# Kernel optimization log

Measured on AMD Instinct MI355X. Metric: run time of the kernel, lower is better.

## Reference

```python
import jax, jax.numpy as jnp
import numpy as np

NEG_SLOPE = 0.2  # PyG GATConv default negative_slope


def gat_conv(x, edge_index, W, a_src, a_dst, bias, heads, out_ch, concat):
    """PyG-style GATConv (eval mode, add_self_loops=True).
    x: [N, F_in], edge_index: [2, E] (row 0 = src, row 1 = dst).
    """
    N = x.shape[0]
    loop = jnp.arange(N, dtype=edge_index.dtype)
    src = jnp.concatenate([edge_index[0], loop])  # [E+N]
    dst = jnp.concatenate([edge_index[1], loop])

    h = (x @ W).reshape(N, heads, out_ch)            # [N, H, C]
    alpha_s = jnp.einsum('nhc,hc->nh', h, a_src)     # [N, H]
    alpha_d = jnp.einsum('nhc,hc->nh', h, a_dst)

    e = jax.nn.leaky_relu(alpha_s[src] + alpha_d[dst], NEG_SLOPE)  # [E+N, H]
    # softmax over incoming edges per destination node (numerically stable)
    m = jax.ops.segment_max(e, dst, num_segments=N)                # [N, H]
    ex = jnp.exp(e - m[dst])
    denom = jax.ops.segment_sum(ex, dst, num_segments=N)
    alpha = ex / (denom[dst] + 1e-16)                              # [E+N, H]

    msg = h[src] * alpha[:, :, None]                               # [E+N, H, C]
    out = jax.ops.segment_sum(msg, dst, num_segments=N)            # [N, H, C]
    out = out.reshape(N, heads * out_ch) if concat else out.mean(axis=1)
    return out + bias


def setup_inputs() -> dict:
    key = jax.random.key(0)
    ks = jax.random.split(key, 10)
    N, F_in, H, C1, LAT, E = 10000, 2000, 10, 128, 64, 150000
    hid = H * C1  # 1280
    x = jax.random.normal(ks[0], (N, F_in), dtype=jnp.float32)
    edge_index = jax.random.randint(ks[1], (2, E), 0, N, dtype=jnp.int64)
    # layer 1 params (glorot-ish scaling)
    W1 = jax.random.normal(ks[2], (F_in, H * C1), dtype=jnp.float32) * (1.0 / np.sqrt(F_in))
    a_src1 = jax.random.normal(ks[3], (H, C1), dtype=jnp.float32) * 0.1
    a_dst1 = jax.random.normal(ks[4], (H, C1), dtype=jnp.float32) * 0.1
    b1 = jnp.zeros((hid,), dtype=jnp.float32)
    # layer 2 params
    W2 = jax.random.normal(ks[5], (hid, H * LAT), dtype=jnp.float32) * (1.0 / np.sqrt(hid))
    a_src2 = jax.random.normal(ks[6], (H, LAT), dtype=jnp.float32) * 0.1
    a_dst2 = jax.random.normal(ks[7], (H, LAT), dtype=jnp.float32) * 0.1
    b2 = jnp.zeros((LAT,), dtype=jnp.float32)
    return {"x": x, "edge_index": edge_index,
            "W1": W1, "a_src1": a_src1, "a_dst1": a_dst1, "b1": b1,
            "W2": W2, "a_src2": a_src2, "a_dst2": a_dst2, "b2": b2}


def reference(x, edge_index, W1, a_src1, a_dst1, b1, W2, a_src2, a_dst2, b2):
    H, C1, LAT = 10, 128, 64
    h1 = gat_conv(x, edge_index, W1, a_src1, a_dst1, b1, H, C1, concat=True)
    h1 = jax.nn.relu(h1)
    h2 = gat_conv(h1, edge_index, W2, a_src2, a_dst2, b2, H, LAT, concat=False)
    return jax.nn.relu(h2)
```

## Files before the change

### kernel.cpp

```cpp
#include <hip/hip_runtime.h>

#define NN    10000
#define FIN   2000
#define NH    10
#define C1    128
#define C2    64
#define HC1   1280
#define HC2   640
#define MP    10240
#define K1P   2016
#define CAP   96

typedef _Float16 f16x8 __attribute__((ext_vector_type(8)));
typedef _Float16 f16x4 __attribute__((ext_vector_type(4)));
typedef _Float16 f16x2 __attribute__((ext_vector_type(2)));
typedef float    f32x4 __attribute__((ext_vector_type(4)));

__device__ __forceinline__ float leaky(float x) { return x > 0.f ? x : 0.2f * x; }

#define NCAST (2 * MP)
#define NW1   (63 * 40)
__global__ void k_prep(const float* __restrict__ x, _Float16* __restrict__ A1,
                       const float* __restrict__ W1, _Float16* __restrict__ W1t) {
    __shared__ float tile[32][33];
    int bid = blockIdx.x, t = threadIdx.x;
    if (bid < NCAST) {
        int r = bid >> 1;
        int c = (bid & 1) * 256 + t;
        if (c >= K1P / 4) return;
        float4 v = make_float4(0.f, 0.f, 0.f, 0.f);
        if (r < NN && c < FIN / 4) v = *(const float4*)(x + (long)r * FIN + 4 * c);
        f16x4 o = {(_Float16)v.x, (_Float16)v.y, (_Float16)v.z, (_Float16)v.w};
        *(f16x4*)(A1 + (long)r * K1P + 4 * c) = o;
        return;
    }
    int i = bid - NCAST;
    int kbase = (i % 63) * 32, nbase = (i / 63) * 32;
    int tx = t & 31, ty = t >> 5;
#pragma unroll
    for (int j = 0; j < 4; j++) {
        int k = kbase + ty + j * 8;
        float v = (k < FIN) ? W1[(long)k * HC1 + nbase + tx] : 0.0f;
        tile[ty + j * 8][tx] = v;
    }
    __syncthreads();
#pragma unroll
    for (int j = 0; j < 4; j++) {
        int n = nbase + ty + j * 8;
        W1t[(long)n * K1P + kbase + tx] = (_Float16)tile[tx][ty + j * 8];
    }
}

__device__ __forceinline__ void gl2lds16(const void* g, void* l) {
    __builtin_amdgcn_global_load_lds((const __attribute__((address_space(1))) void*)g,
                                     (__attribute__((address_space(3))) void*)l, 16, 0, 0);
}

__global__ __launch_bounds__(512, 2) void k_gemm1(const _Float16* __restrict__ A,
                                                  const _Float16* __restrict__ Bt,
                                                  _Float16* __restrict__ C,
                                                  const float* __restrict__ asf,
                                                  const float* __restrict__ adf,
                                                  float* __restrict__ as,
                                                  float* __restrict__ ad,
                                                  const float* __restrict__ W2,
                                                  _Float16* __restrict__ W2t,
                                                  const int* __restrict__ ei,
                                                  int* __restrict__ cnt,
                                                  int* __restrict__ bucket,
                                                  int E, int nblk, int fillb) {
    constexpr int K    = K1P;
    constexpr int N    = HC1;
    constexpr int TBUF = 256 * 32;
    __shared__ char smem[3 * TBUF * 2 * 2] __attribute__((aligned(16)));
    _Float16* As = (_Float16*)smem;
    _Float16* Bs = (_Float16*)(smem + 3 * TBUF * 2);

    int bid = blockIdx.x;
    int t = threadIdx.x;
    if (bid >= nblk) {
        int sb = bid - nblk;
        if (sb < fillb) {
            int i = sb * 512 + t;
            if (i < E + NN) {
                int s, d;
                if (i < E) { s = ei[i]; d = ei[E + i]; }
                else       { s = i - E; d = i - E; }
                int slot = atomicAdd(&cnt[d], 1);
                if (slot < CAP) bucket[d * CAP + slot] = s;
            }
            return;
        }
        int half = t >> 8, t256 = t & 255;
        int i2 = (sb - fillb) * 2 + half;
        int kbase = (i2 % 40) * 32, nbase = (i2 / 40) * 32;
        float* tile = (float*)smem + half * (32 * 33);
        int tx = t256 & 31, ty = t256 >> 5;
#pragma unroll
        for (int j = 0; j < 4; j++) {
            int k = kbase + ty + j * 8;
            tile[(ty + j * 8) * 33 + tx] = W2[(long)k * HC2 + nbase + tx];
        }
        __syncthreads();
#pragma unroll
        for (int j = 0; j < 4; j++) {
            int n = nbase + ty + j * 8;
            W2t[(long)n * HC1 + kbase + tx] = (_Float16)tile[tx * 33 + ty + j * 8];
        }
        return;
    }

    int r = bid & 7, qb = bid >> 3;
    int n_t = qb % 5;
    int m_t = r + 8 * (qb / 5);
    int m0 = m_t * 256;
    int n0 = n_t * 256;
    int lane = t & 63, wave = t >> 6;
    int wr = wave >> 2, wc = wave & 3;
    int lrow = lane & 15, q = lane >> 4;

    f32x4 acc[8][4] = {};

    int sS[2];
#pragma unroll
    for (int i = 0; i < 2; i++) sS[i] = t + 512 * i;
    const _Float16* Ar[2];
    const _Float16* Br[2];
#pragma unroll
    for (int i = 0; i < 2; i++) {
        int row = sS[i] >> 2, gq = (sS[i] & 3) ^ ((sS[i] >> 3) & 3);
        Ar[i] = A  + (long)(m0 + row) * K + gq * 8;
        Br[i] = Bt + (long)(n0 + row) * K + gq * 8;
    }

    int aoff[8], boff[4];
#pragma unroll
    for (int i = 0; i < 8; i++) {
        int rowa = wr * 128 + i * 16 + lrow;
        aoff[i] = rowa * 32 + ((q ^ ((rowa >> 1) & 3)) << 3);
    }
#pragma unroll
    for (int i = 0; i < 4; i++) {
        int rowb = wc * 64 + i * 16 + lrow;
        boff[i] = rowb * 32 + ((q ^ ((rowb >> 1) & 3)) << 3);
    }

    auto stage = [&](int it, int buf) {
        int k0 = it << 5;
#pragma unroll
        for (int i = 0; i < 2; i++) gl2lds16(Ar[i] + k0, &As[buf * TBUF + sS[i] * 8]);
#pragma unroll
        for (int i = 0; i < 2; i++) gl2lds16(Br[i] + k0, &Bs[buf * TBUF + sS[i] * 8]);
    };

    constexpr int WVM = 0x0F70 | 4;
    int nk = K >> 5;
    stage(0, 0);
    stage(1, 1);
    int cur = 0;
    for (int it = 0; it < nk; it++) {
        if (it + 1 < nk) __builtin_amdgcn_s_waitcnt(WVM);
        else             __builtin_amdgcn_s_waitcnt(0x0F70);
        __builtin_amdgcn_s_barrier();
        int nxt = cur + 2; if (nxt >= 3) nxt -= 3;
        if (it + 2 < nk) stage(it + 2, nxt);

        f16x8 af[8], bf[4];
#pragma unroll
        for (int i = 0; i < 8; i++) af[i] = *(const f16x8*)&As[cur * TBUF + aoff[i]];
#pragma unroll
        for (int i = 0; i < 4; i++) bf[i] = *(const f16x8*)&Bs[cur * TBUF + boff[i]];
#pragma unroll
        for (int mt = 0; mt < 8; mt++)
#pragma unroll
            for (int nt = 0; nt < 4; nt++)
                acc[mt][nt] = __builtin_amdgcn_mfma_f32_16x16x32_f16(bf[nt], af[mt], acc[mt][nt], 0, 0, 0);
        cur = (cur + 1 == 3) ? 0 : cur + 1;
    }

#pragma unroll
    for (int mt = 0; mt < 8; mt++) {
        int m = m0 + wr * 128 + mt * 16 + lrow;
#pragma unroll
        for (int nt = 0; nt < 4; nt++) {
            int n = n0 + wc * 64 + nt * 16 + q * 4;
            f16x4 o = {(_Float16)acc[mt][nt][0], (_Float16)acc[mt][nt][1],
                       (_Float16)acc[mt][nt][2], (_Float16)acc[mt][nt][3]};
            *(f16x4*)(C + (long)m * N + n) = o;
        }
    }

    float4 av[4], dvv[4];
#pragma unroll
    for (int nt = 0; nt < 4; nt++) {
        av[nt]  = *(const float4*)(asf + n0 + wc * 64 + nt * 16 + q * 4);
        dvv[nt] = *(const float4*)(adf + n0 + wc * 64 + nt * 16 + q * 4);
    }
    __syncthreads();
    float* sAs = (float*)smem;
    float* sAd = (float*)smem + 1024;
#pragma unroll
    for (int mt = 0; mt < 8; mt++) {
        float ps = 0.f, pd = 0.f;
#pragma unroll
        for (int nt = 0; nt < 4; nt++) {
            ps += acc[mt][nt][0] * av[nt].x + acc[mt][nt][1] * av[nt].y
                + acc[mt][nt][2] * av[nt].z + acc[mt][nt][3] * av[nt].w;
            pd += acc[mt][nt][0] * dvv[nt].x + acc[mt][nt][1] * dvv[nt].y
                + acc[mt][nt][2] * dvv[nt].z + acc[mt][nt][3] * dvv[nt].w;
        }
        ps += __shfl_xor(ps, 16); ps += __shfl_xor(ps, 32);
        pd += __shfl_xor(pd, 16); pd += __shfl_xor(pd, 32);
        if (q == 0) {
            int rl = wr * 128 + mt * 16 + lrow;
            sAs[rl * 4 + wc] = ps;
            sAd[rl * 4 + wc] = pd;
        }
    }
    __syncthreads();
    if (t < 256) {
        int m = m0 + t;
        if (m < NN) {
            int hb = n0 >> 7;
            as[m * NH + hb]     = sAs[t * 4 + 0] + sAs[t * 4 + 1];
            as[m * NH + hb + 1] = sAs[t * 4 + 2] + sAs[t * 4 + 3];
            ad[m * NH + hb]     = sAd[t * 4 + 0] + sAd[t * 4 + 1];
            ad[m * NH + hb + 1] = sAd[t * 4 + 2] + sAd[t * 4 + 3];
        }
    }
}

template<int MFRAG>
__global__ __launch_bounds__(256, 3) void k_gemm(const _Float16* __restrict__ A,
                                                 const _Float16* __restrict__ Bt,
                                                 _Float16* __restrict__ C, int K, int N,
                                                 int NTN,
                                                 const float* __restrict__ asf,
                                                 const float* __restrict__ adf,
                                                 float* __restrict__ as,
                                                 float* __restrict__ ad,
                                                 int headw) {
    constexpr int BM   = MFRAG * 32;
    constexpr int ABUF = BM * 32;
    constexpr int ASL  = BM / 64;
    constexpr int WVM  = 0x0F70 | (ASL + 2);
    __shared__ char smem[3 * ABUF * 2 + 3 * 8192] __attribute__((aligned(16)));
    _Float16* As = (_Float16*)smem;
    _Float16* Bs = (_Float16*)(smem + 3 * ABUF * 2);

    int bid = blockIdx.x;
    int r = bid & 7, qb = bid >> 3;
    int n_t = qb % NTN;
    int m_t = r + 8 * (qb / NTN);
    int m0 = m_t * BM;
    int n0 = n_t * 128;
    int t = threadIdx.x;
    int lane = t & 63, wave = t >> 6;
    int wr = wave >> 1, wc = wave & 1;
    int lrow = lane & 15, q = lane >> 4;

    f32x4 acc[MFRAG][4] = {};

    int sA[ASL], sB[2];
#pragma unroll
    for (int i = 0; i < ASL; i++) sA[i] = t + 256 * i;
#pragma unroll
    for (int i = 0; i < 2; i++) sB[i] = t + 256 * i;
    const _Float16* Ar[ASL];
    const _Float16* Br[2];
#pragma unroll
    for (int i = 0; i < ASL; i++) {
        int row = sA[i] >> 2, gq = (sA[i] & 3) ^ ((sA[i] >> 3) & 3);
        Ar[i] = A + (long)(m0 + row) * K + gq * 8;
    }
#pragma unroll
    for (int i = 0; i < 2; i++) {
        int row = sB[i] >> 2, gq = (sB[i] & 3) ^ ((sB[i] >> 3) & 3);
        Br[i] = Bt + (long)(n0 + row) * K + gq * 8;
    }

    int aoff[MFRAG], boff[4];
#pragma unroll
    for (int i = 0; i < MFRAG; i++) {
        int rowa = wr * (MFRAG * 16) + i * 16 + lrow;
        aoff[i] = rowa * 32 + ((q ^ ((rowa >> 1) & 3)) << 3);
    }
#pragma unroll
    for (int i = 0; i < 4; i++) {
        int rowb = wc * 64 + i * 16 + lrow;
        boff[i] = rowb * 32 + ((q ^ ((rowb >> 1) & 3)) << 3);
    }

    auto stage = [&](int it, int buf) {
        int k0 = it << 5;
#pragma unroll
        for (int i = 0; i < ASL; i++) gl2lds16(Ar[i] + k0, &As[buf * ABUF + sA[i] * 8]);
#pragma unroll
        for (int i = 0; i < 2; i++) gl2lds16(Br[i] + k0, &Bs[buf * 4096 + sB[i] * 8]);
    };

    int nk = K >> 5;
    stage(0, 0);
    stage(1, 1);
    int cur = 0;
    for (int it = 0; it < nk; it++) {
        if (it + 1 < nk) __builtin_amdgcn_s_waitcnt(WVM);
        else             __builtin_amdgcn_s_waitcnt(0x0F70);
        __builtin_amdgcn_s_barrier();
        int nxt = cur + 2; if (nxt >= 3) nxt -= 3;
        if (it + 2 < nk) stage(it + 2, nxt);

        f16x8 af[MFRAG], bf[4];
#pragma unroll
        for (int i = 0; i < MFRAG; i++) af[i] = *(const f16x8*)&As[cur * ABUF + aoff[i]];
#pragma unroll
        for (int i = 0; i < 4; i++) bf[i] = *(const f16x8*)&Bs[cur * 4096 + boff[i]];
#pragma unroll
        for (int mt = 0; mt < MFRAG; mt++)
#pragma unroll
            for (int nt = 0; nt < 4; nt++)
                acc[mt][nt] = __builtin_amdgcn_mfma_f32_16x16x32_f16(bf[nt], af[mt], acc[mt][nt], 0, 0, 0);
        cur = (cur + 1 == 3) ? 0 : cur + 1;
    }

#pragma unroll
    for (int mt = 0; mt < MFRAG; mt++) {
        int m = m0 + wr * (MFRAG * 16) + mt * 16 + lrow;
#pragma unroll
        for (int nt = 0; nt < 4; nt++) {
            int n = n0 + wc * 64 + nt * 16 + q * 4;
            f16x4 o = {(_Float16)acc[mt][nt][0], (_Float16)acc[mt][nt][1],
                       (_Float16)acc[mt][nt][2], (_Float16)acc[mt][nt][3]};
            *(f16x4*)(C + (long)m * N + n) = o;
        }
    }

    float4 av[4], dvv[4];
#pragma unroll
    for (int nt = 0; nt < 4; nt++) {
        av[nt]  = *(const float4*)(asf + n0 + wc * 64 + nt * 16 + q * 4);
        dvv[nt] = *(const float4*)(adf + n0 + wc * 64 + nt * 16 + q * 4);
    }
    __syncthreads();
    float* sAs = (float*)smem;
    float* sAd = (float*)smem + BM * 2;
#pragma unroll
    for (int mt = 0; mt < MFRAG; mt++) {
        float ps = 0.f, pd = 0.f;
#pragma unroll
        for (int nt = 0; nt < 4; nt++) {
            ps += acc[mt][nt][0] * av[nt].x + acc[mt][nt][1] * av[nt].y
                + acc[mt][nt][2] * av[nt].z + acc[mt][nt][3] * av[nt].w;
            pd += acc[mt][nt][0] * dvv[nt].x + acc[mt][nt][1] * dvv[nt].y
                + acc[mt][nt][2] * dvv[nt].z + acc[mt][nt][3] * dvv[nt].w;
        }
        ps += __shfl_xor(ps, 16); ps += __shfl_xor(ps, 32);
        pd += __shfl_xor(pd, 16); pd += __shfl_xor(pd, 32);
        if (q == 0) {
            int rl = wr * (MFRAG * 16) + mt * 16 + lrow;
            sAs[rl * 2 + wc] = ps;
            sAd[rl * 2 + wc] = pd;
        }
    }
    __syncthreads();
    if (t < BM) {
        int m = m0 + t;
        if (m < NN) {
            int hb = n0 / headw;
            if (headw == 128) {
                as[m * NH + hb] = sAs[t * 2] + sAs[t * 2 + 1];
                ad[m * NH + hb] = sAd[t * 2] + sAd[t * 2 + 1];
            } else {
                as[m * NH + hb]     = sAs[t * 2];
                as[m * NH + hb + 1] = sAs[t * 2 + 1];
                ad[m * NH + hb]     = sAd[t * 2];
                ad[m * NH + hb + 1] = sAd[t * 2 + 1];
            }
        }
    }
}

__global__ __launch_bounds__(320) void k_agg1(const int* __restrict__ cnt,
                                              const int* __restrict__ bucket,
                                              const float* __restrict__ as,
                                              const float* __restrict__ ad,
                                              const _Float16* __restrict__ h,
                                              const float* __restrict__ bias,
                                              _Float16* __restrict__ A2) {
    __shared__ int sidx[64];
    __shared__ float sal[64 * NH];
    int n = blockIdx.x, t = threadIdx.x;
    if (n >= NN) {
        f16x4 z = {(_Float16)0.f, (_Float16)0.f, (_Float16)0.f, (_Float16)0.f};
        *(f16x4*)(A2 + (long)n * HC1 + 4 * t) = z;
        return;
    }
    int deg = min(cnt[n], CAP);
    const int* bkt = bucket + (long)n * CAP;
    int w = t >> 6, lane = t & 63;
    int hd = t >> 5;
    float acc[4] = {0, 0, 0, 0};

    if (deg <= 64) {
        int src = (lane < deg) ? bkt[lane] : 0;
        float2 adv = *(const float2*)(ad + n * NH + 2 * w);
        float x0 = 0.f, x1 = 0.f;
        if (lane < deg) {
            float2 avv = *(const float2*)(as + (long)src * NH + 2 * w);
            x0 = __expf(leaky(avv.x + adv.x));
            x1 = __expf(leaky(avv.y + adv.y));
        }
        float s0 = x0, s1 = x1;
        for (int m = 32; m; m >>= 1) {
            s0 += __shfl_xor(s0, m);
            s1 += __shfl_xor(s1, m);
        }
        if (lane < deg) {
            sal[lane * NH + 2 * w]     = x0 / (s0 + 1e-16f);
            sal[lane * NH + 2 * w + 1] = x1 / (s1 + 1e-16f);
            if (w == 0) sidx[lane] = src;
        }
        __syncthreads();
        int j = 0;
        for (; j + 8 <= deg; j += 8) {
            int sj[8]; float aa[8];
#pragma unroll
            for (int u = 0; u < 8; u++) { sj[u] = sidx[j + u]; aa[u] = sal[(j + u) * NH + hd]; }
            f16x4 vv[8];
#pragma unroll
            for (int u = 0; u < 8; u++) vv[u] = *(const f16x4*)(h + (long)sj[u] * HC1 + 4 * t);
#pragma unroll
            for (int i = 0; i < 4; i++) {
                float s = 0.f;
#pragma unroll
                for (int u = 0; u < 8; u++) s += aa[u] * (float)vv[u][i];
                acc[i] += s;
            }
        }
        for (; j + 4 <= deg; j += 4) {
            int sj0 = sidx[j], sj1 = sidx[j + 1], sj2 = sidx[j + 2], sj3 = sidx[j + 3];
            float a0 = sal[j * NH + hd], a1 = sal[(j + 1) * NH + hd];
            float a2 = sal[(j + 2) * NH + hd], a3 = sal[(j + 3) * NH + hd];
            f16x4 v0 = *(const f16x4*)(h + (long)sj0 * HC1 + 4 * t);
            f16x4 v1 = *(const f16x4*)(h + (long)sj1 * HC1 + 4 * t);
            f16x4 v2 = *(const f16x4*)(h + (long)sj2 * HC1 + 4 * t);
            f16x4 v3 = *(const f16x4*)(h + (long)sj3 * HC1 + 4 * t);
#pragma unroll
            for (int i = 0; i < 4; i++)
                acc[i] += a0 * (float)v0[i] + a1 * (float)v1[i]
                        + a2 * (float)v2[i] + a3 * (float)v3[i];
        }
        for (; j < deg; j++) {
            int src2 = sidx[j];
            float a = sal[j * NH + hd];
            f16x4 v = *(const f16x4*)(h + (long)src2 * HC1 + 4 * t);
#pragma unroll
            for (int i = 0; i < 4; i++) acc[i] += a * (float)v[i];
        }
    } else {
        float2 adv = *(const float2*)(ad + n * NH + 2 * w);
        float s0 = 0.f, s1 = 0.f;
        for (int j = lane; j < deg; j += 64) {
            float2 avv = *(const float2*)(as + (long)bkt[j] * NH + 2 * w);
            s0 += __expf(leaky(avv.x + adv.x));
            s1 += __expf(leaky(avv.y + adv.y));
        }
        for (int m = 32; m; m >>= 1) {
            s0 += __shfl_xor(s0, m);
            s1 += __shfl_xor(s1, m);
        }
        float i0 = 1.f / (s0 + 1e-16f), i1 = 1.f / (s1 + 1e-16f);
        for (int c0 = 0; c0 < deg; c0 += 64) {
            int cn = min(64, deg - c0);
            __syncthreads();
            if (lane < cn) {
                int src = bkt[c0 + lane];
                float2 avv = *(const float2*)(as + (long)src * NH + 2 * w);
                sal[lane * NH + 2 * w]     = __expf(leaky(avv.x + adv.x)) * i0;
                sal[lane * NH + 2 * w + 1] = __expf(leaky(avv.y + adv.y)) * i1;
                if (w == 0) sidx[lane] = src;
            }
            __syncthreads();
            for (int j = 0; j < cn; j++) {
                int src2 = sidx[j];
                float a = sal[j * NH + hd];
                f16x4 v = *(const f16x4*)(h + (long)src2 * HC1 + 4 * t);
#pragma unroll
                for (int i = 0; i < 4; i++) acc[i] += a * (float)v[i];
            }
        }
    }
    f16x4 o;
#pragma unroll
    for (int i = 0; i < 4; i++) {
        float x = acc[i] + bias[4 * t + i];
        o[i] = (_Float16)(x > 0.f ? x : 0.f);
    }
    *(f16x4*)(A2 + (long)n * HC1 + 4 * t) = o;
}

__global__ __launch_bounds__(320) void k_agg2(const int* __restrict__ cnt,
                                              const int* __restrict__ bucket,
                                              const float* __restrict__ as,
                                              const float* __restrict__ ad,
                                              const _Float16* __restrict__ h,
                                              const float* __restrict__ bias,
                                              float* __restrict__ out) {
    __shared__ int sidx[64];
    __shared__ float sal[64 * NH];
    __shared__ float facc[HC2];
    int n = blockIdx.x, t = threadIdx.x;
    int deg = min(cnt[n], CAP);
    const int* bkt = bucket + (long)n * CAP;
    int w = t >> 6, lane = t & 63;
    int hd = t >> 5;
    float a0 = 0.f, a1 = 0.f;

    if (deg <= 64) {
        int src = (lane < deg) ? bkt[lane] : 0;
        float2 adv = *(const float2*)(ad + n * NH + 2 * w);
        float x0 = 0.f, x1 = 0.f;
        if (lane < deg) {
            float2 avv = *(const float2*)(as + (long)src * NH + 2 * w);
            x0 = __expf(leaky(avv.x + adv.x));
            x1 = __expf(leaky(avv.y + adv.y));
        }
        float s0 = x0, s1 = x1;
        for (int m = 32; m; m >>= 1) {
            s0 += __shfl_xor(s0, m);
            s1 += __shfl_xor(s1, m);
        }
        if (lane < deg) {
            sal[lane * NH + 2 * w]     = x0 / (s0 + 1e-16f);
            sal[lane * NH + 2 * w + 1] = x1 / (s1 + 1e-16f);
            if (w == 0) sidx[lane] = src;
        }
        __syncthreads();
        int j = 0;
        for (; j + 8 <= deg; j += 8) {
            int sj[8]; float aa[8];
#pragma unroll
            for (int u = 0; u < 8; u++) { sj[u] = sidx[j + u]; aa[u] = sal[(j + u) * NH + hd]; }
            f16x2 vv[8];
#pragma unroll
            for (int u = 0; u < 8; u++) vv[u] = *(const f16x2*)(h + (long)sj[u] * HC2 + 2 * t);
            float p0 = 0.f, p1 = 0.f;
#pragma unroll
            for (int u = 0; u < 8; u++) { p0 += aa[u] * (float)vv[u][0]; p1 += aa[u] * (float)vv[u][1]; }
            a0 += p0; a1 += p1;
        }
        for (; j + 4 <= deg; j += 4) {
            int sj0 = sidx[j], sj1 = sidx[j + 1], sj2 = sidx[j + 2], sj3 = sidx[j + 3];
            float b0 = sal[j * NH + hd], b1 = sal[(j + 1) * NH + hd];
            float b2 = sal[(j + 2) * NH + hd], b3 = sal[(j + 3) * NH + hd];
            f16x2 v0 = *(const f16x2*)(h + (long)sj0 * HC2 + 2 * t);
            f16x2 v1 = *(const f16x2*)(h + (long)sj1 * HC2 + 2 * t);
            f16x2 v2 = *(const f16x2*)(h + (long)sj2 * HC2 + 2 * t);
            f16x2 v3 = *(const f16x2*)(h + (long)sj3 * HC2 + 2 * t);
            a0 += b0 * (float)v0[0] + b1 * (float)v1[0] + b2 * (float)v2[0] + b3 * (float)v3[0];
            a1 += b0 * (float)v0[1] + b1 * (float)v1[1] + b2 * (float)v2[1] + b3 * (float)v3[1];
        }
        for (; j < deg; j++) {
            int src2 = sidx[j];
            float a = sal[j * NH + hd];
            f16x2 v = *(const f16x2*)(h + (long)src2 * HC2 + 2 * t);
            a0 += a * (float)v[0];
            a1 += a * (float)v[1];
        }
    } else {
        float2 adv = *(const float2*)(ad + n * NH + 2 * w);
        float s0 = 0.f, s1 = 0.f;
        for (int j = lane; j < deg; j += 64) {
            float2 avv = *(const float2*)(as + (long)bkt[j] * NH + 2 * w);
            s0 += __expf(leaky(avv.x + adv.x));
            s1 += __expf(leaky(avv.y + adv.y));
        }
        for (int m = 32; m; m >>= 1) {
            s0 += __shfl_xor(s0, m);
            s1 += __shfl_xor(s1, m);
        }
        float i0 = 1.f / (s0 + 1e-16f), i1 = 1.f / (s1 + 1e-16f);
        for (int c0 = 0; c0 < deg; c0 += 64) {
            int cn = min(64, deg - c0);
            __syncthreads();
            if (lane < cn) {
                int src = bkt[c0 + lane];
                float2 avv = *(const float2*)(as + (long)src * NH + 2 * w);
                sal[lane * NH + 2 * w]     = __expf(leaky(avv.x + adv.x)) * i0;
                sal[lane * NH + 2 * w + 1] = __expf(leaky(avv.y + adv.y)) * i1;
                if (w == 0) sidx[lane] = src;
            }
            __syncthreads();
            for (int j = 0; j < cn; j++) {
                int src2 = sidx[j];
                float a = sal[j * NH + hd];
                f16x2 v = *(const f16x2*)(h + (long)src2 * HC2 + 2 * t);
                a0 += a * (float)v[0];
                a1 += a * (float)v[1];
            }
        }
    }
    facc[2 * t] = a0;
    facc[2 * t + 1] = a1;
    __syncthreads();
    if (t < C2) {
        float s = 0.f;
#pragma unroll
        for (int hh = 0; hh < NH; hh++) s += facc[hh * C2 + t];
        s = s * 0.1f + bias[t];
        out[(long)n * C2 + t] = s > 0.f ? s : 0.f;
    }
}

extern "C" void kernel_launch(void* const* d_in, const int* in_sizes, int n_in,
                              void* d_out, int out_size, void* d_ws, size_t ws_size,
                              hipStream_t stream) {
    const float* x      = (const float*)d_in[0];
    const int*   ei     = (const int*)d_in[1];
    const float* W1     = (const float*)d_in[2];
    const float* asrc1  = (const float*)d_in[3];
    const float* adst1  = (const float*)d_in[4];
    const float* b1     = (const float*)d_in[5];
    const float* W2     = (const float*)d_in[6];
    const float* asrc2  = (const float*)d_in[7];
    const float* adst2  = (const float*)d_in[8];
    const float* b2     = (const float*)d_in[9];
    float* out = (float*)d_out;
    const int E  = in_sizes[1] / 2;

    char* base = (char*)d_ws;
    size_t o = 0;
    auto alloc = [&](size_t bytes) { size_t r = o; o += (bytes + 255) & ~(size_t)255; return r; };
    _Float16* A1    = (_Float16*)(base + alloc((size_t)MP * K1P * 2));
    _Float16* W1t   = (_Float16*)(base + alloc((size_t)HC1 * K1P * 2));
    _Float16* A2    = (_Float16*)(base + alloc((size_t)MP * HC1 * 2));
    _Float16* W2t   = (_Float16*)(base + alloc((size_t)HC2 * HC1 * 2));
    _Float16* h1pre = (_Float16*)(base + alloc((size_t)MP * HC1 * 2));
    _Float16* h2pre = (_Float16*)(base + alloc((size_t)MP * HC2 * 2));
    float* as1      = (float*)(base + alloc((size_t)NN * NH * 4));
    float* ad1      = (float*)(base + alloc((size_t)NN * NH * 4));
    float* as2      = (float*)(base + alloc((size_t)NN * NH * 4));
    float* ad2      = (float*)(base + alloc((size_t)NN * NH * 4));
    int* cnt        = (int*)(base + alloc((size_t)NN * 4));
    int* bucket     = (int*)(base + alloc((size_t)NN * CAP * 4));
    (void)ws_size; (void)n_in; (void)out_size;

    const int FILLB = (E + NN + 511) / 512;
    const int W2TB  = (40 * 20) / 2;
    const int G1 = 8 * (MP / 256 / 8) * (HC1 / 256);
    const int G2 = 8 * (MP / 256 / 8) * (HC2 / 128);

    hipMemsetAsync(cnt, 0, (size_t)NN * 4, stream);
    k_prep<<<NCAST + NW1, 256, 0, stream>>>(x, A1, W1, W1t);
    k_gemm1<<<G1 + FILLB + W2TB, 512, 0, stream>>>(A1, W1t, h1pre, asrc1, adst1, as1, ad1,
                                                   W2, W2t, ei, cnt, bucket, E, G1, FILLB);
    k_agg1<<<MP, 320, 0, stream>>>(cnt, bucket, as1, ad1, h1pre, b1, A2);
    k_gemm<8><<<G2, 256, 0, stream>>>(A2, W2t, h2pre, HC1, HC2, HC2 / 128,
                                      asrc2, adst2, as2, ad2, C2);
    k_agg2<<<NN, 320, 0, stream>>>(cnt, bucket, as2, ad2, h2pre, b2, out);
}
```

Before: 327.9 us.

## Split edge aggregation across two thread groups with wider vector loads

Both aggregation kernels now split the 320 threads into two groups of 160. Each group handles alternate neighbor edges and loads wider fp16 vectors (8 halves per thread in layer 1, 4 in layer 2). The two partial sums are combined through shared memory before the bias and ReLU epilogue. This is meant to cut the number of memory instructions per gathered row and raise memory-level parallelism, at the cost of extra shared memory and a block-wide sync. The second GEMM is also switched to a smaller M-tile template (k_gemm<4>) with a doubled grid, which should improve occupancy and load balance.

```diff
diff --git a/kernel.cpp b/kernel.cpp
--- a/kernel.cpp
+++ b/kernel.cpp
@@ -389,6 +389,7 @@
                                               _Float16* __restrict__ A2) {
     __shared__ int sidx[64];
     __shared__ float sal[64 * NH];
+    __shared__ float sacc[2][HC1];
     int n = blockIdx.x, t = threadIdx.x;
     if (n >= NN) {
         f16x4 z = {(_Float16)0.f, (_Float16)0.f, (_Float16)0.f, (_Float16)0.f};
@@ -398,8 +399,10 @@
     int deg = min(cnt[n], CAP);
     const int* bkt = bucket + (long)n * CAP;
     int w = t >> 6, lane = t & 63;
-    int hd = t >> 5;
-    float acc[4] = {0, 0, 0, 0};
+    int g = (t >= 160) ? 1 : 0;
+    int c = t - 160 * g;
+    int hd8 = c >> 4;
+    float acc8[8] = {};
 
     if (deg <= 64) {
         int src = (lane < deg) ? bkt[lane] : 0;
@@ -423,39 +426,33 @@
         __syncthreads();
         int j = 0;
         for (; j + 8 <= deg; j += 8) {
-            int sj[8]; float aa[8];
-#pragma unroll
-            for (int u = 0; u < 8; u++) { sj[u] = sidx[j + u]; aa[u] = sal[(j + u) * NH + hd]; }
-            f16x4 vv[8];
-#pragma unroll
-            for (int u = 0; u < 8; u++) vv[u] = *(const f16x4*)(h + (long)sj[u] * HC1 + 4 * t);
-#pragma unroll
-            for (int i = 0; i < 4; i++) {
-                float s = 0.f;
-#pragma unroll
-                for (int u = 0; u < 8; u++) s += aa[u] * (float)vv[u][i];
-                acc[i] += s;
-            }
-        }
-        for (; j + 4 <= deg; j += 4) {
-            int sj0 = sidx[j], sj1 = sidx[j + 1], sj2 = sidx[j + 2], sj3 = sidx[j + 3];
-            float a0 = sal[j * NH + hd], a1 = sal[(j + 1) * NH + hd];
-            float a2 = sal[(j + 2) * NH + hd], a3 = sal[(j + 3) * NH + hd];
-            f16x4 v0 = *(const f16x4*)(h + (long)sj0 * HC1 + 4 * t);
-            f16x4 v1 = *(const f16x4*)(h + (long)sj1 * HC1 + 4 * t);
-            f16x4 v2 = *(const f16x4*)(h + (long)sj2 * HC1 + 4 * t);
-            f16x4 v3 = *(const f16x4*)(h + (long)sj3 * HC1 + 4 * t);
-#pragma unroll
-            for (int i = 0; i < 4; i++)
-                acc[i] += a0 * (float)v0[i] + a1 * (float)v1[i]
-                        + a2 * (float)v2[i] + a3 * (float)v3[i];
-        }
-        for (; j < deg; j++) {
-            int src2 = sidx[j];
-            float a = sal[j * NH + hd];
-            f16x4 v = *(const f16x4*)(h + (long)src2 * HC1 + 4 * t);
-#pragma unroll
-            for (int i = 0; i < 4; i++) acc[i] += a * (float)v[i];
+            int r0 = j + g, r1 = j + 2 + g, r2 = j + 4 + g, r3 = j + 6 + g;
+            int s0i = sidx[r0], s1i = sidx[r1], s2i = sidx[r2], s3i = sidx[r3];
+            float a0 = sal[r0 * NH + hd8], a1 = sal[r1 * NH + hd8];
+            float a2 = sal[r2 * NH + hd8], a3 = sal[r3 * NH + hd8];
+            f16x8 v0 = *(const f16x8*)(h + (long)s0i * HC1 + 8 * c);
+            f16x8 v1 = *(const f16x8*)(h + (long)s1i * HC1 + 8 * c);
+            f16x8 v2 = *(const f16x8*)(h + (long)s2i * HC1 + 8 * c);
+            f16x8 v3 = *(const f16x8*)(h + (long)s3i * HC1 + 8 * c);
+#pragma unroll
+            for (int i = 0; i < 8; i++)
+                acc8[i] += a0 * (float)v0[i] + a1 * (float)v1[i]
+                         + a2 * (float)v2[i] + a3 * (float)v3[i];
+        }
+        for (; j + 2 <= deg; j += 2) {
+            int rr = j + g;
+            int ss = sidx[rr];
+            float aa = sal[rr * NH + hd8];
+            f16x8 v = *(const f16x8*)(h + (long)ss * HC1 + 8 * c);
+#pragma unroll
+            for (int i = 0; i < 8; i++) acc8[i] += aa * (float)v[i];
+        }
+        if (j < deg && g == 0) {
+            int ss = sidx[j];
+            float aa = sal[j * NH + hd8];
+            f16x8 v = *(const f16x8*)(h + (long)ss * HC1 + 8 * c);
+#pragma unroll
+            for (int i = 0; i < 8; i++) acc8[i] += aa * (float)v[i];
         }
     } else {
         float2 adv = *(const float2*)(ad + n * NH + 2 * w);
@@ -481,19 +478,32 @@
                 if (w == 0) sidx[lane] = src;
             }
             __syncthreads();
-            for (int j = 0; j < cn; j++) {
-                int src2 = sidx[j];
-                float a = sal[j * NH + hd];
-                f16x4 v = *(const f16x4*)(h + (long)src2 * HC1 + 4 * t);
-#pragma unroll
-                for (int i = 0; i < 4; i++) acc[i] += a * (float)v[i];
-            }
-        }
-    }
+            int jj = 0;
+            for (; jj + 2 <= cn; jj += 2) {
+                int rr = jj + g;
+                int ss = sidx[rr];
+                float aa = sal[rr * NH + hd8];
+                f16x8 v = *(const f16x8*)(h + (long)ss * HC1 + 8 * c);
+#pragma unroll
+                for (int i = 0; i < 8; i++) acc8[i] += aa * (float)v[i];
+            }
+            if (jj < cn && g == 0) {
+                int ss = sidx[jj];
+                float aa = sal[jj * NH + hd8];
+                f16x8 v = *(const f16x8*)(h + (long)ss * HC1 + 8 * c);
+#pragma unroll
+                for (int i = 0; i < 8; i++) acc8[i] += aa * (float)v[i];
+            }
+        }
+    }
+#pragma unroll
+    for (int i = 0; i < 8; i++) sacc[g][8 * c + i] = acc8[i];
+    __syncthreads();
     f16x4 o;
 #pragma unroll
     for (int i = 0; i < 4; i++) {
-        float x = acc[i] + bias[4 * t + i];
+        int ch = 4 * t + i;
+        float x = sacc[0][ch] + sacc[1][ch] + bias[ch];
         o[i] = (_Float16)(x > 0.f ? x : 0.f);
     }
     *(f16x4*)(A2 + (long)n * HC1 + 4 * t) = o;
@@ -508,13 +518,15 @@
                                               float* __restrict__ out) {
     __shared__ int sidx[64];
     __shared__ float sal[64 * NH];
-    __shared__ float facc[HC2];
+    __shared__ float sacc[2][HC2];
     int n = blockIdx.x, t = threadIdx.x;
     int deg = min(cnt[n], CAP);
     const int* bkt = bucket + (long)n * CAP;
     int w = t >> 6, lane = t & 63;
-    int hd = t >> 5;
-    float a0 = 0.f, a1 = 0.f;
+    int g = (t >= 160) ? 1 : 0;
+    int c = t - 160 * g;
+    int hd4 = c >> 4;
+    float acc4[4] = {};
 
     if (deg <= 64) {
         int src = (lane < deg) ? bkt[lane] : 0;
@@ -538,34 +550,33 @@
         __syncthreads();
         int j = 0;
         for (; j + 8 <= deg; j += 8) {
-            int sj[8]; float aa[8];
-#pragma unroll
-            for (int u = 0; u < 8; u++) { sj[u] = sidx[j + u]; aa[u] = sal[(j + u) * NH + hd]; }
-            f16x2 vv[8];
-#pragma unroll
-            for (int u = 0; u < 8; u++) vv[u] = *(const f16x2*)(h + (long)sj[u] * HC2 + 2 * t);
-            float p0 = 0.f, p1 = 0.f;
-#pragma unroll
-            for (int u = 0; u < 8; u++) { p0 += aa[u] * (float)vv[u][0]; p1 += aa[u] * (float)vv[u][1]; }
-            a0 += p0; a1 += p1;
-        }
-        for (; j + 4 <= deg; j += 4) {
-            int sj0 = sidx[j], sj1 = sidx[j + 1], sj2 = sidx[j + 2], sj3 = sidx[j + 3];
-            float b0 = sal[j * NH + hd], b1 = sal[(j + 1) * NH + hd];
-            float b2 = sal[(j + 2) * NH + hd], b3 = sal[(j + 3) * NH + hd];
-            f16x2 v0 = *(const f16x2*)(h + (long)sj0 * HC2 + 2 * t);
-            f16x2 v1 = *(const f16x2*)(h + (long)sj1 * HC2 + 2 * t);
-            f16x2 v2 = *(const f16x2*)(h + (long)sj2 * HC2 + 2 * t);
-            f16x2 v3 = *(const f16x2*)(h + (long)sj3 * HC2 + 2 * t);
-            a0 += b0 * (float)v0[0] + b1 * (float)v1[0] + b2 * (float)v2[0] + b3 * (float)v3[0];
-            a1 += b0 * (float)v0[1] + b1 * (float)v1[1] + b2 * (float)v2[1] + b3 * (float)v3[1];
-        }
-        for (; j < deg; j++) {
-            int src2 = sidx[j];
-            float a = sal[j * NH + hd];
-            f16x2 v = *(const f16x2*)(h + (long)src2 * HC2 + 2 * t);
-            a0 += a * (float)v[0];
-            a1 += a * (float)v[1];
+            int r0 = j + g, r1 = j + 2 + g, r2 = j + 4 + g, r3 = j + 6 + g;
+            int s0i = sidx[r0], s1i = sidx[r1], s2i = sidx[r2], s3i = sidx[r3];
+            float a0 = sal[r0 * NH + hd4], a1 = sal[r1 * NH + hd4];
+            float a2 = sal[r2 * NH + hd4], a3 = sal[r3 * NH + hd4];
+            f16x4 v0 = *(const f16x4*)(h + (long)s0i * HC2 + 4 * c);
+            f16x4 v1 = *(const f16x4*)(h + (long)s1i * HC2 + 4 * c);
+            f16x4 v2 = *(const f16x4*)(h + (long)s2i * HC2 + 4 * c);
+            f16x4 v3 = *(const f16x4*)(h + (long)s3i * HC2 + 4 * c);
+#pragma unroll
+            for (int i = 0; i < 4; i++)
+                acc4[i] += a0 * (float)v0[i] + a1 * (float)v1[i]
+                         + a2 * (float)v2[i] + a3 * (float)v3[i];
+        }
+        for (; j + 2 <= deg; j += 2) {
+            int rr = j + g;
+            int ss = sidx[rr];
+            float aa = sal[rr * NH + hd4];
+            f16x4 v = *(const f16x4*)(h + (long)ss * HC2 + 4 * c);
+#pragma unroll
+            for (int i = 0; i < 4; i++) acc4[i] += aa * (float)v[i];
+        }
+        if (j < deg && g == 0) {
+            int ss = sidx[j];
+            float aa = sal[j * NH + hd4];
+            f16x4 v = *(const f16x4*)(h + (long)ss * HC2 + 4 * c);
+#pragma unroll
+            for (int i = 0; i < 4; i++) acc4[i] += aa * (float)v[i];
         }
     } else {
         float2 adv = *(const float2*)(ad + n * NH + 2 * w);
@@ -591,22 +602,37 @@
                 if (w == 0) sidx[lane] = src;
             }
             __syncthreads();
-            for (int j = 0; j < cn; j++) {
-                int src2 = sidx[j];
-                float a = sal[j * NH + hd];
-                f16x2 v = *(const f16x2*)(h + (long)src2 * HC2 + 2 * t);
-                a0 += a * (float)v[0];
-                a1 += a * (float)v[1];
-            }
-        }
-    }
-    facc[2 * t] = a0;
-    facc[2 * t + 1] = a1;
+            int jj = 0;
+            for (; jj + 2 <= cn; jj += 2) {
+                int rr = jj + g;
+                int ss = sidx[rr];
+                float aa = sal[rr * NH + hd4];
+                f16x4 v = *(const f16x4*)(h + (long)ss * HC2 + 4 * c);
+#pragma unroll
+                for (int i = 0; i < 4; i++) acc4[i] += aa * (float)v[i];
+            }
+            if (jj < cn && g == 0) {
+                int ss = sidx[jj];
+                float aa = sal[jj * NH + hd4];
+                f16x4 v = *(const f16x4*)(h + (long)ss * HC2 + 4 * c);
+#pragma unroll
+                for (int i = 0; i < 4; i++) acc4[i] += aa * (float)v[i];
+            }
+        }
+    }
+#pragma unroll
+    for (int i = 0; i < 4; i++) sacc[g][4 * c + i] = acc4[i];
+    __syncthreads();
+    if (t < 320) {
+        int ch = 2 * t;
+        sacc[0][ch]     += sacc[1][ch];
+        sacc[0][ch + 1] += sacc[1][ch + 1];
+    }
     __syncthreads();
     if (t < C2) {
         float s = 0.f;
 #pragma unroll
-        for (int hh = 0; hh < NH; hh++) s += facc[hh * C2 + t];
+        for (int hh = 0; hh < NH; hh++) s += sacc[0][hh * C2 + t];
         s = s * 0.1f + bias[t];
         out[(long)n * C2 + t] = s > 0.f ? s : 0.f;
     }
@@ -648,14 +674,14 @@
     const int FILLB = (E + NN + 511) / 512;
     const int W2TB  = (40 * 20) / 2;
     const int G1 = 8 * (MP / 256 / 8) * (HC1 / 256);
-    const int G2 = 8 * (MP / 256 / 8) * (HC2 / 128);
+    const int G2 = 8 * (MP / 128 / 8) * (HC2 / 128);
 
     hipMemsetAsync(cnt, 0, (size_t)NN * 4, stream);
     k_prep<<<NCAST + NW1, 256, 0, stream>>>(x, A1, W1, W1t);
     k_gemm1<<<G1 + FILLB + W2TB, 512, 0, stream>>>(A1, W1t, h1pre, asrc1, adst1, as1, ad1,
                                                    W2, W2t, ei, cnt, bucket, E, G1, FILLB);
     k_agg1<<<MP, 320, 0, stream>>>(cnt, bucket, as1, ad1, h1pre, b1, A2);
-    k_gemm<8><<<G2, 256, 0, stream>>>(A2, W2t, h2pre, HC1, HC2, HC2 / 128,
+    k_gemm<4><<<G2, 256, 0, stream>>>(A2, W2t, h2pre, HC1, HC2, HC2 / 128,
                                       asrc2, adst2, as2, ad2, C2);
     k_agg2<<<NN, 320, 0, stream>>>(cnt, bucket, as2, ad2, h2pre, b2, out);
 }
```

New measurement: 331.8 us. About the same (+1.2%).
